# Kernel optimization log

Measured on AMD Instinct MI355X. Metric: run time of the kernel, lower is better.

## Reference

```python
import jax, jax.numpy as jnp
from jax import lax
import numpy as np

B, H, W, C = 2, 256, 256, 256
HEADS, DH = 8, 32  # C == HEADS * DH


def _dwconv(x, w, pad):
    # x: [B,C,H,W], w: [C,1,kh,kw] depthwise (feature_group_count=C)
    return lax.conv_general_dilated(
        x, w, window_strides=(1, 1), padding=[(pad, pad), (pad, pad)],
        dimension_numbers=('NCHW', 'OIHW', 'NCHW'), feature_group_count=x.shape[1])


def _conv1x1(x, w, b):
    # x: [B,C,H,W], w: [Cout,Cin], b: [Cout]
    return jnp.einsum('bchw,oc->bohw', x, w) + b[None, :, None, None]


def _l2norm(x, axis=-1, eps=1e-12):
    # matches F.normalize: x / max(||x||, eps)
    n = jnp.sqrt(jnp.sum(x * x, axis=axis, keepdims=True))
    return x / jnp.maximum(n, eps)


def setup_inputs():
    key = jax.random.key(0)
    ks = jax.random.split(key, 16)
    s = 0.02
    f32 = jnp.float32
    return {
        'x_in': jax.random.normal(ks[0], (B, H, W, C), f32),
        'mask': jax.random.uniform(ks[1], (B, H, W, C), f32),
        'wq': jax.random.normal(ks[2], (C, C), f32) * s,
        'wk': jax.random.normal(ks[3], (C, C), f32) * s,
        'wv': jax.random.normal(ks[4], (C, C), f32) * s,
        'rescale': jnp.ones((HEADS, 1, 1), f32),
        'proj_w': jax.random.normal(ks[5], (C, C), f32) * s,
        'proj_b': jnp.zeros((C,), f32),
        'pos_w1': jax.random.normal(ks[6], (C, 1, 3, 3), f32) * s,
        'pos_w2': jax.random.normal(ks[7], (C, 1, 3, 3), f32) * s,
        'mm_c1_w': jax.random.normal(ks[8], (C, C), f32) * s,
        'mm_c1_b': jnp.zeros((C,), f32),
        'mm_c2_w': jax.random.normal(ks[9], (C, C), f32) * s,
        'mm_c2_b': jnp.zeros((C,), f32),
        'mm_dw_w': jax.random.normal(ks[10], (C, 1, 5, 5), f32) * s,
        'mm_dw_b': jnp.zeros((C,), f32),
    }


def reference(x_in, mask, wq, wk, wv, rescale, proj_w, proj_b, pos_w1, pos_w2,
              mm_c1_w, mm_c1_b, mm_c2_w, mm_c2_b, mm_dw_w, mm_dw_b):
    b, h, w, c = x_in.shape
    n = h * w
    x = x_in.reshape(b, n, c)

    # q, k, v: [b, heads, n, dh]
    def split_heads(t):
        return t.reshape(b, n, HEADS, DH).transpose(0, 2, 1, 3)
    q = split_heads(x @ wq)
    k = split_heads(x @ wk)
    v = split_heads(x @ wv)

    # MaskGuidedMechanism on NCHW mask
    m = _conv1x1(mask.transpose(0, 3, 1, 2), mm_c1_w, mm_c1_b)          # [b,c,h,w]
    attn_map = jax.nn.sigmoid(_dwconv(_conv1x1(m, mm_c2_w, mm_c2_b), mm_dw_w, 2)
                              + mm_dw_b[None, :, None, None])
    m = m * attn_map + m                                                 # [b,c,h,w]
    mask_attn = split_heads(m.transpose(0, 2, 3, 1).reshape(b, n, c))    # [b,heads,n,dh]

    v = v * mask_attn

    # transpose to channel-attention layout: [b, heads, dh, n]
    q = _l2norm(q.transpose(0, 1, 3, 2))
    k = _l2norm(k.transpose(0, 1, 3, 2))
    v = v.transpose(0, 1, 3, 2)

    attn = jnp.einsum('bhdn,bhen->bhde', k, q) * rescale  # [b,heads,dh,dh]
    attn = jax.nn.softmax(attn, axis=-1)
    out = jnp.einsum('bhde,bhen->bhdn', attn, v)          # [b,heads,dh,n]
    out = out.transpose(0, 3, 1, 2).reshape(b, n, c)      # [b,n,c]
    out_c = (out @ proj_w + proj_b).reshape(b, h, w, c)

    # positional embedding: two depthwise 3x3 convs with exact GELU between
    p = _dwconv(x_in.transpose(0, 3, 1, 2), pos_w1, 1)
    p = jax.nn.gelu(p, approximate=False)
    p = _dwconv(p, pos_w2, 1)
    out_p = p.transpose(0, 2, 3, 1)

    return out_c + out_p
```

## Files before the change

### kernel.cpp

```cpp
#include <hip/hip_runtime.h>
#include <math.h>

#define CCH 256
#define HEADS 8
#define DHH 32
#define BATCH 2
#define HDIM 256
#define WDIM 256
#define NPIX (HDIM*WDIM)
#define PTOT (BATCH*NPIX)
#define GCH 64

typedef __attribute__((ext_vector_type(8))) short bfrag;
typedef __attribute__((ext_vector_type(4))) float ffrag;

__device__ __forceinline__ unsigned short f2bf(float f) {
  unsigned u = __builtin_bit_cast(unsigned, f);
  u += 0x7fffu + ((u >> 16) & 1u);
  return (unsigned short)(u >> 16);
}
__device__ __forceinline__ float bf2f(unsigned short h) {
  unsigned u = (unsigned)h << 16;
  return __builtin_bit_cast(float, u);
}

__global__ __launch_bounds__(256) void gemm_mfma(
    const float* __restrict__ A, const float* __restrict__ Wt,
    const float* __restrict__ bias, const float* __restrict__ emul,
    float* __restrict__ C)
{
  __shared__ unsigned short AsH[128][40];
  __shared__ unsigned short AsL[128][40];
  __shared__ unsigned short WsH[128][40];
  __shared__ unsigned short WsL[128][40];
  const int t = threadIdx.x;
  const int m0 = blockIdx.x * 128;
  const int n0 = blockIdx.y * 128;
  const int lane = t & 63;
  const int wave = t >> 6;
  const int wr = (wave >> 1) * 64;
  const int wc = (wave & 1) * 64;
  const int sr = t >> 1;
  const int sk = (t & 1) * 16;

  ffrag acc[4][4];
  #pragma unroll
  for (int i = 0; i < 4; ++i)
    #pragma unroll
    for (int j = 0; j < 4; ++j)
      acc[i][j] = (ffrag)0.f;

  const int fr = lane & 15;
  const int kc = (lane >> 4) * 8;

  for (int k0 = 0; k0 < 256; k0 += 32) {
    const float* ap = A  + (size_t)(m0 + sr) * 256 + k0 + sk;
    const float* wp = Wt + (size_t)(n0 + sr) * 256 + k0 + sk;
    float4 av[4], wv4[4];
    #pragma unroll
    for (int s = 0; s < 4; ++s) {
      av[s]  = *(const float4*)(ap + s*4);
      wv4[s] = *(const float4*)(wp + s*4);
    }
    __syncthreads();
    #pragma unroll
    for (int s = 0; s < 4; ++s) {
      const float* a4 = (const float*)&av[s];
      const float* w4 = (const float*)&wv4[s];
      #pragma unroll
      for (int p = 0; p < 4; p += 2) {
        unsigned short h0 = f2bf(a4[p]), h1 = f2bf(a4[p+1]);
        unsigned short l0 = f2bf(a4[p]   - bf2f(h0));
        unsigned short l1 = f2bf(a4[p+1] - bf2f(h1));
        *(unsigned*)&AsH[sr][sk + s*4 + p] = (unsigned)h0 | ((unsigned)h1 << 16);
        *(unsigned*)&AsL[sr][sk + s*4 + p] = (unsigned)l0 | ((unsigned)l1 << 16);
        unsigned short g0 = f2bf(w4[p]), g1 = f2bf(w4[p+1]);
        unsigned short e0 = f2bf(w4[p]   - bf2f(g0));
        unsigned short e1 = f2bf(w4[p+1] - bf2f(g1));
        *(unsigned*)&WsH[sr][sk + s*4 + p] = (unsigned)g0 | ((unsigned)g1 << 16);
        *(unsigned*)&WsL[sr][sk + s*4 + p] = (unsigned)e0 | ((unsigned)e1 << 16);
      }
    }
    __syncthreads();
    bfrag ah[4], alo[4], bh[4], blo[4];
    #pragma unroll
    for (int i = 0; i < 4; ++i) {
      ah[i]  = *(const bfrag*)&AsH[wr + i*16 + fr][kc];
      alo[i] = *(const bfrag*)&AsL[wr + i*16 + fr][kc];
      bh[i]  = *(const bfrag*)&WsH[wc + i*16 + fr][kc];
      blo[i] = *(const bfrag*)&WsL[wc + i*16 + fr][kc];
    }
    #pragma unroll
    for (int i = 0; i < 4; ++i)
      #pragma unroll
      for (int j = 0; j < 4; ++j) {
        acc[i][j] = __builtin_amdgcn_mfma_f32_16x16x32_bf16(ah[i],  bh[j],  acc[i][j], 0, 0, 0);
        acc[i][j] = __builtin_amdgcn_mfma_f32_16x16x32_bf16(ah[i],  blo[j], acc[i][j], 0, 0, 0);
        acc[i][j] = __builtin_amdgcn_mfma_f32_16x16x32_bf16(alo[i], bh[j],  acc[i][j], 0, 0, 0);
      }
  }

  const int er = (lane >> 4) * 4;
  const int ec = lane & 15;
  #pragma unroll
  for (int i = 0; i < 4; ++i) {
    #pragma unroll
    for (int j = 0; j < 4; ++j) {
      #pragma unroll
      for (int q = 0; q < 4; ++q) {
        int grow = m0 + wr + i*16 + er + q;
        int gcol = n0 + wc + j*16 + ec;
        size_t idx = (size_t)grow * 256 + gcol;
        float o = acc[i][j][q];
        if (emul) o *= emul[idx];
        if (bias) o += bias[gcol];
        C[idx] = o;
      }
    }
  }
}

__global__ __launch_bounds__(256) void transpose256(
    const float* __restrict__ src, float* __restrict__ dst)
{
  __shared__ float tile[32][33];
  const int bx = blockIdx.x & 7, by = blockIdx.x >> 3;
  const int tx = threadIdx.x & 31, ty = threadIdx.x >> 5;
  #pragma unroll
  for (int s = 0; s < 32; s += 8)
    tile[ty + s][tx] = src[(by*32 + ty + s)*256 + bx*32 + tx];
  __syncthreads();
  #pragma unroll
  for (int s = 0; s < 32; s += 8)
    dst[(bx*32 + ty + s)*256 + by*32 + tx] = tile[tx][ty + s];
}

__global__ __launch_bounds__(256) void syrk_partial(
    const float* __restrict__ X, float* __restrict__ Gp)
{
  __shared__ float xi[64][68];
  __shared__ float xj[64][68];
  const int TI[10] = {0,0,0,0,1,1,1,2,2,3};
  const int TJ[10] = {0,1,2,3,1,2,3,2,3,3};
  const int t = threadIdx.x;
  int blk = blockIdx.x;
  const int pair  = blk % 10;
  const int chunk = (blk / 10) % GCH;
  const int b     = blk / (10 * GCH);
  const int ti = TI[pair], tj = TJ[pair];
  const size_t xb = (size_t)b * NPIX * CCH;
  const int n0 = chunk * (NPIX / GCH);
  const int lr = t >> 2;
  const int lc = (t & 3) * 16;
  const int iy = (t >> 4) * 4;
  const int jx = (t & 15) * 4;
  float acc[4][4] = {};

  for (int pt = 0; pt < (NPIX / GCH) / 64; ++pt) {
    const float* xr = X + xb + (size_t)(n0 + pt*64 + lr) * 256;
    float4 vi[4], vj[4];
    #pragma unroll
    for (int s = 0; s < 4; ++s) {
      vi[s] = *(const float4*)(xr + ti*64 + lc + s*4);
      vj[s] = *(const float4*)(xr + tj*64 + lc + s*4);
    }
    __syncthreads();
    #pragma unroll
    for (int s = 0; s < 4; ++s) {
      *(float4*)&xi[lr][lc + s*4] = vi[s];
      *(float4*)&xj[lr][lc + s*4] = vj[s];
    }
    __syncthreads();
    #pragma unroll 8
    for (int p = 0; p < 64; ++p) {
      float av[4], bv[4];
      *(float4*)&av[0] = *(const float4*)&xi[p][iy];
      *(float4*)&bv[0] = *(const float4*)&xj[p][jx];
      #pragma unroll
      for (int i = 0; i < 4; ++i)
        #pragma unroll
        for (int j = 0; j < 4; ++j)
          acc[i][j] += av[i] * bv[j];
    }
  }
  float* g = Gp + (size_t)(b * GCH + chunk) * 65536;
  #pragma unroll
  for (int i = 0; i < 4; ++i)
    #pragma unroll
    for (int j = 0; j < 4; ++j)
      g[(ti*64 + iy + i) * 256 + (tj*64 + jx + j)] = acc[i][j];
}

__global__ __launch_bounds__(256) void syrk_reduce(
    const float* __restrict__ Gp, float* __restrict__ G)
{
  int flat = blockIdx.x * 256 + threadIdx.x;
  int b  = flat >> 16;
  int ij = flat & 65535;
  int i = ij >> 8, j = ij & 255;
  int src = ((i >> 6) <= (j >> 6)) ? (i*256 + j) : (j*256 + i);
  float s = 0.f;
  for (int ch = 0; ch < GCH; ++ch)
    s += Gp[(size_t)(b*GCH + ch) * 65536 + src];
  G[(size_t)b * 65536 + ij] = s;
}

__global__ __launch_bounds__(256) void headS_kernel(
    const float* __restrict__ wk, const float* __restrict__ TQ,
    float* __restrict__ S)
{
  __shared__ float wks[256][32];
  __shared__ float tqs[256][32];
  const int t  = threadIdx.x;
  const int bh = blockIdx.x;
  const int b = bh >> 3, h = bh & 7;
  const float* wkrow = wk + (size_t)t * 256 + h*32;
  const float* tqrow = TQ + (size_t)b * 65536 + (size_t)t * 256 + h*32;
  #pragma unroll
  for (int e = 0; e < 32; ++e) {
    wks[t][(e + t) & 31] = wkrow[e];
    tqs[t][(e + t) & 31] = tqrow[e];
  }
  __syncthreads();
  const int d  = t >> 3;
  const int e0 = (t & 7) * 4;
  float acc[4] = {0.f, 0.f, 0.f, 0.f};
  for (int c1 = 0; c1 < 256; ++c1) {
    float kv = wks[c1][(d + c1) & 31];
    #pragma unroll
    for (int j = 0; j < 4; ++j)
      acc[j] += kv * tqs[c1][(e0 + j + c1) & 31];
  }
  #pragma unroll
  for (int j = 0; j < 4; ++j)
    S[bh*1024 + d*32 + e0 + j] = acc[j];
}

__global__ __launch_bounds__(256) void norms_part(
    const float* __restrict__ wq, const float* __restrict__ wk,
    const float* __restrict__ TQ, const float* __restrict__ TK,
    float* __restrict__ nqp, float* __restrict__ nkp)
{
  const int o = threadIdx.x;
  const int ch = blockIdx.x & 7;
  const int b  = blockIdx.x >> 3;
  float sq = 0.f, sk = 0.f;
  for (int c1 = ch*32; c1 < ch*32 + 32; ++c1) {
    sq += wq[c1*256 + o] * TQ[(size_t)b*65536 + c1*256 + o];
    sk += wk[c1*256 + o] * TK[(size_t)b*65536 + c1*256 + o];
  }
  nqp[(b*8 + ch)*256 + o] = sq;
  nkp[(b*8 + ch)*256 + o] = sk;
}

__global__ __launch_bounds__(256) void norms_comb(
    const float* __restrict__ nqp, const float* __restrict__ nkp,
    float* __restrict__ nq, float* __restrict__ nk)
{
  int flat = blockIdx.x * 256 + threadIdx.x;
  int b = flat >> 8, o = flat & 255;
  float sq = 0.f, sk = 0.f;
  #pragma unroll
  for (int ch = 0; ch < 8; ++ch) {
    sq += nqp[(b*8 + ch)*256 + o];
    sk += nkp[(b*8 + ch)*256 + o];
  }
  nq[flat] = sq;
  nk[flat] = sk;
}

__global__ __launch_bounds__(64) void attn_final(
    const float* __restrict__ S, const float* __restrict__ nq,
    const float* __restrict__ nk, const float* __restrict__ rescale,
    float* __restrict__ attn)
{
  const int bh = blockIdx.x;
  const int b = bh >> 3, h = bh & 7;
  const int d = threadIdx.x;
  if (d >= 32) return;
  const float r = rescale[h];
  const float nkd = fmaxf(sqrtf(nk[b*256 + h*32 + d]), 1e-12f);
  float vals[32];
  float mx = -1e30f;
  #pragma unroll
  for (int e = 0; e < 32; ++e) {
    float nqe = fmaxf(sqrtf(nq[b*256 + h*32 + e]), 1e-12f);
    float x = S[bh*1024 + d*32 + e] / (nkd * nqe) * r;
    vals[e] = x;
    mx = fmaxf(mx, x);
  }
  float sum = 0.f;
  #pragma unroll
  for (int e = 0; e < 32; ++e) { vals[e] = expf(vals[e] - mx); sum += vals[e]; }
  float inv = 1.f / sum;
  #pragma unroll
  for (int e = 0; e < 32; ++e) attn[bh*1024 + d*32 + e] = vals[e] * inv;
}

__global__ __launch_bounds__(256) void fold_proj(
    const float* __restrict__ attn, const float* __restrict__ projw,
    float* __restrict__ WbT)
{
  const int o  = threadIdx.x;
  const int he = blockIdx.x & 255;
  const int b  = blockIdx.x >> 8;
  const int h = he >> 5, e = he & 31;
  float acc = 0.f;
  #pragma unroll
  for (int d = 0; d < 32; ++d)
    acc += attn[((b*8 + h)*32 + d)*32 + e] * projw[(h*32 + d)*256 + o];
  WbT[(size_t)b*65536 + (size_t)o*256 + he] = acc;
}

__global__ __launch_bounds__(256) void mgm_kernel(
    const float* __restrict__ tin, float* __restrict__ m,
    const float* __restrict__ dww, const float* __restrict__ dwb)
{
  const int c  = threadIdx.x;
  const int blk = blockIdx.x;
  const int xc = (blk & 7) * 32;
  const int y  = (blk >> 3) & 255;
  const int b  = blk >> 11;
  float w[25];
  #pragma unroll
  for (int i = 0; i < 25; ++i) w[i] = dww[c*25 + i];
  const float bias = dwb[c];
  const float* base = tin + (size_t)b * NPIX * CCH + c;
  int yo[5];
  #pragma unroll
  for (int dy = 0; dy < 5; ++dy) {
    int yy = y + dy - 2;
    yo[dy] = (yy >= 0 && yy <= 255) ? yy * 65536 : -1;
  }
  float col[5][5];
  #pragma unroll
  for (int j = 0; j < 4; ++j) {
    int xx = xc - 2 + j;
    bool xv = (xx >= 0 && xx <= 255);
    #pragma unroll
    for (int dy = 0; dy < 5; ++dy)
      col[j][dy] = (xv && yo[dy] >= 0) ? base[yo[dy] + xx*256] : 0.f;
  }
  size_t mi = (size_t)b * NPIX * CCH + ((size_t)y*256 + xc)*256 + c;
  #pragma unroll 4
  for (int xi = 0; xi < 32; ++xi) {
    int xx = xc + xi + 2;
    bool xv = (xx <= 255);
    #pragma unroll
    for (int dy = 0; dy < 5; ++dy)
      col[4][dy] = (xv && yo[dy] >= 0) ? base[yo[dy] + xx*256] : 0.f;
    float conv = 0.f;
    #pragma unroll
    for (int dy = 0; dy < 5; ++dy)
      #pragma unroll
      for (int j = 0; j < 5; ++j)
        conv += col[j][dy] * w[dy*5 + j];
    float sig = 1.f / (1.f + expf(-(conv + bias)));
    m[mi] = m[mi] * (1.f + sig);
    mi += 256;
    #pragma unroll
    for (int j = 0; j < 4; ++j)
      #pragma unroll
      for (int dy = 0; dy < 5; ++dy)
        col[j][dy] = col[j+1][dy];
  }
}

__global__ __launch_bounds__(256) void pos1_kernel(
    const float* __restrict__ xin, const float* __restrict__ w1,
    float* __restrict__ p1)
{
  const int c  = threadIdx.x;
  const int blk = blockIdx.x;
  const int xc = (blk & 7) * 32;
  const int y  = (blk >> 3) & 255;
  const int b  = blk >> 11;
  float w[9];
  #pragma unroll
  for (int i = 0; i < 9; ++i) w[i] = w1[c*9 + i];
  const float* base = xin + (size_t)b * NPIX * CCH + c;
  int yo[3];
  #pragma unroll
  for (int dy = 0; dy < 3; ++dy) {
    int yy = y + dy - 1;
    yo[dy] = (yy >= 0 && yy <= 255) ? yy * 65536 : -1;
  }
  float col[3][3];
  #pragma unroll
  for (int j = 0; j < 2; ++j) {
    int xx = xc - 1 + j;
    bool xv = (xx >= 0 && xx <= 255);
    #pragma unroll
    for (int dy = 0; dy < 3; ++dy)
      col[j][dy] = (xv && yo[dy] >= 0) ? base[yo[dy] + xx*256] : 0.f;
  }
  size_t pi = (size_t)b * NPIX * CCH + ((size_t)y*256 + xc)*256 + c;
  #pragma unroll 4
  for (int xi = 0; xi < 32; ++xi) {
    int xx = xc + xi + 1;
    bool xv = (xx <= 255);
    #pragma unroll
    for (int dy = 0; dy < 3; ++dy)
      col[2][dy] = (xv && yo[dy] >= 0) ? base[yo[dy] + xx*256] : 0.f;
    float conv = 0.f;
    #pragma unroll
    for (int dy = 0; dy < 3; ++dy)
      #pragma unroll
      for (int j = 0; j < 3; ++j)
        conv += col[j][dy] * w[dy*3 + j];
    float g = 0.5f * conv * (1.f + erff(conv * 0.70710678118654752f));
    p1[pi] = g;
    pi += 256;
    #pragma unroll
    for (int j = 0; j < 2; ++j)
      #pragma unroll
      for (int dy = 0; dy < 3; ++dy)
        col[j][dy] = col[j+1][dy];
  }
}

__global__ __launch_bounds__(256) void pos2_kernel(
    const float* __restrict__ p1, const float* __restrict__ w2,
    float* __restrict__ out)
{
  const int c  = threadIdx.x;
  const int blk = blockIdx.x;
  const int xc = (blk & 7) * 32;
  const int y  = (blk >> 3) & 255;
  const int b  = blk >> 11;
  float w[9];
  #pragma unroll
  for (int i = 0; i < 9; ++i) w[i] = w2[c*9 + i];
  const float* base = p1 + (size_t)b * NPIX * CCH + c;
  int yo[3];
  #pragma unroll
  for (int dy = 0; dy < 3; ++dy) {
    int yy = y + dy - 1;
    yo[dy] = (yy >= 0 && yy <= 255) ? yy * 65536 : -1;
  }
  float col[3][3];
  #pragma unroll
  for (int j = 0; j < 2; ++j) {
    int xx = xc - 1 + j;
    bool xv = (xx >= 0 && xx <= 255);
    #pragma unroll
    for (int dy = 0; dy < 3; ++dy)
      col[j][dy] = (xv && yo[dy] >= 0) ? base[yo[dy] + xx*256] : 0.f;
  }
  size_t pi = (size_t)b * NPIX * CCH + ((size_t)y*256 + xc)*256 + c;
  #pragma unroll 4
  for (int xi = 0; xi < 32; ++xi) {
    int xx = xc + xi + 1;
    bool xv = (xx <= 255);
    #pragma unroll
    for (int dy = 0; dy < 3; ++dy)
      col[2][dy] = (xv && yo[dy] >= 0) ? base[yo[dy] + xx*256] : 0.f;
    float conv = 0.f;
    #pragma unroll
    for (int dy = 0; dy < 3; ++dy)
      #pragma unroll
      for (int j = 0; j < 3; ++j)
        conv += col[j][dy] * w[dy*3 + j];
    out[pi] = out[pi] + conv;
    pi += 256;
    #pragma unroll
    for (int j = 0; j < 2; ++j)
      #pragma unroll
      for (int dy = 0; dy < 3; ++dy)
        col[j][dy] = col[j+1][dy];
  }
}

extern "C" void kernel_launch(void* const* d_in, const int* in_sizes, int n_in,
                              void* d_out, int out_size, void* d_ws, size_t ws_size,
                              hipStream_t stream)
{
  const float* x_in   = (const float*)d_in[0];
  const float* mask   = (const float*)d_in[1];
  const float* wq     = (const float*)d_in[2];
  const float* wk     = (const float*)d_in[3];
  const float* wv     = (const float*)d_in[4];
  const float* rescal = (const float*)d_in[5];
  const float* proj_w = (const float*)d_in[6];
  const float* proj_b = (const float*)d_in[7];
  const float* pos_w1 = (const float*)d_in[8];
  const float* pos_w2 = (const float*)d_in[9];
  const float* c1w    = (const float*)d_in[10];
  const float* c1b    = (const float*)d_in[11];
  const float* c2w    = (const float*)d_in[12];
  const float* c2b    = (const float*)d_in[13];
  const float* dww    = (const float*)d_in[14];
  const float* dwb    = (const float*)d_in[15];
  float* OUT = (float*)d_out;

  float* A   = (float*)d_ws;
  float* WbT = A + (size_t)PTOT * CCH;

  float* Gp  = OUT;
  float* G   = OUT + 8388608;
  float* TQ  = G   + 131072;
  float* TK  = TQ  + 131072;
  float* S   = TK  + 131072;
  float* nqp = S   + 16384;
  float* nkp = nqp + 4096;
  float* nq  = nkp + 4096;
  float* nk  = nq  + 512;
  float* at  = nk  + 512;
  float* wvT = at  + 16384;
  float* wqT = wvT + 65536;
  float* wkT = wqT + 65536;

  dim3 gg(PTOT / 128, 2);

  gemm_mfma<<<gg, 256, 0, stream>>>(mask, c1w, c1b, nullptr, A);
  gemm_mfma<<<gg, 256, 0, stream>>>(A,    c2w, c2b, nullptr, OUT);
  mgm_kernel<<<4096, 256, 0, stream>>>(OUT, A, dww, dwb);
  transpose256<<<64, 256, 0, stream>>>(wv, wvT);
  transpose256<<<64, 256, 0, stream>>>(wq, wqT);
  transpose256<<<64, 256, 0, stream>>>(wk, wkT);
  syrk_partial<<<2 * GCH * 10, 256, 0, stream>>>(x_in, Gp);
  syrk_reduce<<<512, 256, 0, stream>>>(Gp, G);
  for (int b = 0; b < 2; ++b) {
    gemm_mfma<<<dim3(2,2), 256, 0, stream>>>(G + (size_t)b*65536, wqT, nullptr, nullptr, TQ + (size_t)b*65536);
    gemm_mfma<<<dim3(2,2), 256, 0, stream>>>(G + (size_t)b*65536, wkT, nullptr, nullptr, TK + (size_t)b*65536);
  }
  headS_kernel<<<16, 256, 0, stream>>>(wk, TQ, S);
  norms_part<<<16, 256, 0, stream>>>(wq, wk, TQ, TK, nqp, nkp);
  norms_comb<<<2, 256, 0, stream>>>(nqp, nkp, nq, nk);
  attn_final<<<16, 64, 0, stream>>>(S, nq, nk, rescal, at);
  fold_proj<<<512, 256, 0, stream>>>(at, proj_w, WbT);
  gemm_mfma<<<gg, 256, 0, stream>>>(x_in, wvT, nullptr, A, A);
  {
    dim3 gp(NPIX / 128, 2);
    for (int b = 0; b < 2; ++b)
      gemm_mfma<<<gp, 256, 0, stream>>>(A + (size_t)b * NPIX * CCH,
                                        WbT + (size_t)b * 65536,
                                        proj_b, nullptr,
                                        OUT + (size_t)b * NPIX * CCH);
  }
  pos1_kernel<<<4096, 256, 0, stream>>>(x_in, pos_w1, A);
  pos2_kernel<<<4096, 256, 0, stream>>>(A, pos_w2, OUT);
}
```

Baseline: 1.465 ms.

## Presplit weights to bf16 hi/lo, MFMA Gram kernel, swizzled LDS with prefetch

Weights are now pre-split into bf16 high/low halves by small prep kernels, so the GEMM loads them directly instead of converting each tile. The GEMM gains an XOR-swizzled shared-memory layout and register prefetch of the next K-tile, and splits activations with truncation plus a byte-permute in place of round-to-nearest. The fp32 scalar Gram (x^T x) partial kernel is replaced by a full 256x256 split-bf16 MFMA kernel over 128 chunks, with a vectorized reduce. This trades extra partial-buffer traffic and truncation-based rounding for much higher matrix-core throughput.

```diff
diff --git a/kernel.cpp b/kernel.cpp
--- a/kernel.cpp
+++ b/kernel.cpp
@@ -3,206 +3,239 @@
 
 #define CCH 256
 #define HEADS 8
-#define DHH 32
 #define BATCH 2
-#define HDIM 256
-#define WDIM 256
-#define NPIX (HDIM*WDIM)
-#define PTOT (BATCH*NPIX)
-#define GCH 64
+#define NPIX 65536
+#define PTOT 131072
+#define NCH 128
 
 typedef __attribute__((ext_vector_type(8))) short bfrag;
 typedef __attribute__((ext_vector_type(4))) float ffrag;
-
-__device__ __forceinline__ unsigned short f2bf(float f) {
-  unsigned u = __builtin_bit_cast(unsigned, f);
-  u += 0x7fffu + ((u >> 16) & 1u);
-  return (unsigned short)(u >> 16);
-}
-__device__ __forceinline__ float bf2f(unsigned short h) {
-  unsigned u = (unsigned)h << 16;
+typedef unsigned short u16;
+
+#define KSW(row, g) ((((g) ^ (((row) >> 3) & 3)) << 3))
+
+__device__ __forceinline__ float trunc_bf(float f) {
+  unsigned u = __builtin_bit_cast(unsigned, f) & 0xffff0000u;
   return __builtin_bit_cast(float, u);
 }
+__device__ __forceinline__ unsigned pack_hi(float f0, float f1) {
+  return __builtin_amdgcn_perm(__builtin_bit_cast(unsigned, f1),
+                               __builtin_bit_cast(unsigned, f0), 0x07060302u);
+}
+__device__ __forceinline__ void split2(float f0, float f1, unsigned& h, unsigned& l) {
+  h = pack_hi(f0, f1);
+  l = pack_hi(f0 - trunc_bf(f0), f1 - trunc_bf(f1));
+}
 
 __global__ __launch_bounds__(256) void gemm_mfma(
-    const float* __restrict__ A, const float* __restrict__ Wt,
-    const float* __restrict__ bias, const float* __restrict__ emul,
-    float* __restrict__ C)
-{
-  __shared__ unsigned short AsH[128][40];
-  __shared__ unsigned short AsL[128][40];
-  __shared__ unsigned short WsH[128][40];
-  __shared__ unsigned short WsL[128][40];
+    const float* __restrict__ A, const u16* __restrict__ WH,
+    const u16* __restrict__ WL, const float* __restrict__ bias,
+    const float* __restrict__ emul, float* __restrict__ C)
+{
+  __shared__ u16 AsH[128][40], AsL[128][40], WsH[128][40], WsL[128][40];
   const int t = threadIdx.x;
-  const int m0 = blockIdx.x * 128;
-  const int n0 = blockIdx.y * 128;
-  const int lane = t & 63;
-  const int wave = t >> 6;
-  const int wr = (wave >> 1) * 64;
-  const int wc = (wave & 1) * 64;
+  const int m0 = blockIdx.x * 128, n0 = blockIdx.y * 128;
+  const int lane = t & 63, wave = t >> 6;
+  const int wr = (wave >> 1) * 64, wc = (wave & 1) * 64;
   const int sr = t >> 1;
-  const int sk = (t & 1) * 16;
+  const int g0 = (t & 1) * 2;
+  const int fr = lane & 15, kcg = lane >> 4;
+
+  const float* ap  = A  + (size_t)(m0 + sr) * 256 + g0 * 8;
+  const u16*   whp = WH + (size_t)(n0 + sr) * 256 + g0 * 8;
+  const u16*   wlp = WL + (size_t)(n0 + sr) * 256 + g0 * 8;
 
   ffrag acc[4][4];
   #pragma unroll
   for (int i = 0; i < 4; ++i)
     #pragma unroll
-    for (int j = 0; j < 4; ++j)
-      acc[i][j] = (ffrag)0.f;
-
-  const int fr = lane & 15;
-  const int kc = (lane >> 4) * 8;
+    for (int j = 0; j < 4; ++j) acc[i][j] = (ffrag)0.f;
+
+  float4 av[4]; uint4 whv[2], wlv[2];
+  auto LOADT = [&](int k0) {
+    #pragma unroll
+    for (int s = 0; s < 4; ++s) av[s] = *(const float4*)(ap + k0 + s * 4);
+    whv[0] = *(const uint4*)(whp + k0);
+    whv[1] = *(const uint4*)(whp + k0 + 8);
+    wlv[0] = *(const uint4*)(wlp + k0);
+    wlv[1] = *(const uint4*)(wlp + k0 + 8);
+  };
+  LOADT(0);
 
   for (int k0 = 0; k0 < 256; k0 += 32) {
-    const float* ap = A  + (size_t)(m0 + sr) * 256 + k0 + sk;
-    const float* wp = Wt + (size_t)(n0 + sr) * 256 + k0 + sk;
-    float4 av[4], wv4[4];
+    __syncthreads();
+    unsigned h[8], l[8];
     #pragma unroll
     for (int s = 0; s < 4; ++s) {
-      av[s]  = *(const float4*)(ap + s*4);
-      wv4[s] = *(const float4*)(wp + s*4);
+      split2(av[s].x, av[s].y, h[2*s],   l[2*s]);
+      split2(av[s].z, av[s].w, h[2*s+1], l[2*s+1]);
     }
+    *(uint4*)&AsH[sr][KSW(sr, g0)]     = make_uint4(h[0], h[1], h[2], h[3]);
+    *(uint4*)&AsH[sr][KSW(sr, g0 + 1)] = make_uint4(h[4], h[5], h[6], h[7]);
+    *(uint4*)&AsL[sr][KSW(sr, g0)]     = make_uint4(l[0], l[1], l[2], l[3]);
+    *(uint4*)&AsL[sr][KSW(sr, g0 + 1)] = make_uint4(l[4], l[5], l[6], l[7]);
+    *(uint4*)&WsH[sr][KSW(sr, g0)]     = whv[0];
+    *(uint4*)&WsH[sr][KSW(sr, g0 + 1)] = whv[1];
+    *(uint4*)&WsL[sr][KSW(sr, g0)]     = wlv[0];
+    *(uint4*)&WsL[sr][KSW(sr, g0 + 1)] = wlv[1];
     __syncthreads();
-    #pragma unroll
-    for (int s = 0; s < 4; ++s) {
-      const float* a4 = (const float*)&av[s];
-      const float* w4 = (const float*)&wv4[s];
-      #pragma unroll
-      for (int p = 0; p < 4; p += 2) {
-        unsigned short h0 = f2bf(a4[p]), h1 = f2bf(a4[p+1]);
-        unsigned short l0 = f2bf(a4[p]   - bf2f(h0));
-        unsigned short l1 = f2bf(a4[p+1] - bf2f(h1));
-        *(unsigned*)&AsH[sr][sk + s*4 + p] = (unsigned)h0 | ((unsigned)h1 << 16);
-        *(unsigned*)&AsL[sr][sk + s*4 + p] = (unsigned)l0 | ((unsigned)l1 << 16);
-        unsigned short g0 = f2bf(w4[p]), g1 = f2bf(w4[p+1]);
-        unsigned short e0 = f2bf(w4[p]   - bf2f(g0));
-        unsigned short e1 = f2bf(w4[p+1] - bf2f(g1));
-        *(unsigned*)&WsH[sr][sk + s*4 + p] = (unsigned)g0 | ((unsigned)g1 << 16);
-        *(unsigned*)&WsL[sr][sk + s*4 + p] = (unsigned)e0 | ((unsigned)e1 << 16);
-      }
-    }
-    __syncthreads();
-    bfrag ah[4], alo[4], bh[4], blo[4];
+    if (k0 < 224) LOADT(k0 + 32);
+
+    bfrag ah[4], al_[4], bh[4], bl_[4];
     #pragma unroll
     for (int i = 0; i < 4; ++i) {
-      ah[i]  = *(const bfrag*)&AsH[wr + i*16 + fr][kc];
-      alo[i] = *(const bfrag*)&AsL[wr + i*16 + fr][kc];
-      bh[i]  = *(const bfrag*)&WsH[wc + i*16 + fr][kc];
-      blo[i] = *(const bfrag*)&WsL[wc + i*16 + fr][kc];
+      int ra = wr + i * 16 + fr, rb = wc + i * 16 + fr;
+      ah[i]  = *(const bfrag*)&AsH[ra][KSW(ra, kcg)];
+      al_[i] = *(const bfrag*)&AsL[ra][KSW(ra, kcg)];
+      bh[i]  = *(const bfrag*)&WsH[rb][KSW(rb, kcg)];
+      bl_[i] = *(const bfrag*)&WsL[rb][KSW(rb, kcg)];
     }
     #pragma unroll
     for (int i = 0; i < 4; ++i)
       #pragma unroll
       for (int j = 0; j < 4; ++j) {
         acc[i][j] = __builtin_amdgcn_mfma_f32_16x16x32_bf16(ah[i],  bh[j],  acc[i][j], 0, 0, 0);
-        acc[i][j] = __builtin_amdgcn_mfma_f32_16x16x32_bf16(ah[i],  blo[j], acc[i][j], 0, 0, 0);
-        acc[i][j] = __builtin_amdgcn_mfma_f32_16x16x32_bf16(alo[i], bh[j],  acc[i][j], 0, 0, 0);
+        acc[i][j] = __builtin_amdgcn_mfma_f32_16x16x32_bf16(ah[i],  bl_[j], acc[i][j], 0, 0, 0);
+        acc[i][j] = __builtin_amdgcn_mfma_f32_16x16x32_bf16(al_[i], bh[j],  acc[i][j], 0, 0, 0);
       }
   }
 
-  const int er = (lane >> 4) * 4;
-  const int ec = lane & 15;
-  #pragma unroll
-  for (int i = 0; i < 4; ++i) {
-    #pragma unroll
-    for (int j = 0; j < 4; ++j) {
+  const int er = (lane >> 4) * 4, ec = lane & 15;
+  #pragma unroll
+  for (int i = 0; i < 4; ++i)
+    #pragma unroll
+    for (int j = 0; j < 4; ++j)
       #pragma unroll
       for (int q = 0; q < 4; ++q) {
-        int grow = m0 + wr + i*16 + er + q;
-        int gcol = n0 + wc + j*16 + ec;
+        int grow = m0 + wr + i * 16 + er + q;
+        int gcol = n0 + wc + j * 16 + ec;
         size_t idx = (size_t)grow * 256 + gcol;
         float o = acc[i][j][q];
         if (emul) o *= emul[idx];
         if (bias) o += bias[gcol];
         C[idx] = o;
       }
+}
+
+__global__ __launch_bounds__(512, 2) void syrk_mfma(
+    const float* __restrict__ X, float* __restrict__ Gp)
+{
+  __shared__ u16 XsH[256][40], XsL[256][40];
+  const int t = threadIdx.x;
+  const int blk = blockIdx.x;
+  const int chunk = blk & (NCH - 1);
+  const int b = blk >> 7;
+  const size_t xb = (size_t)b * NPIX * CCH;
+  const int nbase = chunk * (NPIX / NCH);
+  const int lane = t & 63, wave = t >> 6;
+  const int r0 = wave * 32;
+  const int fr = lane & 15, kcg = lane >> 4;
+  const int cw = t & 31;
+  const int n2 = (t >> 5) * 2;
+  const int gst = n2 >> 3, nin = n2 & 7;
+
+  ffrag acc[2][16];
+  #pragma unroll
+  for (int i = 0; i < 2; ++i)
+    #pragma unroll
+    for (int j = 0; j < 16; ++j) acc[i][j] = (ffrag)0.f;
+
+  float fa[8], fb[8];
+  auto LOADT = [&](int it) {
+    const float* xr = X + xb + (size_t)(nbase + it * 32 + n2) * 256 + cw;
+    #pragma unroll
+    for (int j = 0; j < 8; ++j) { fa[j] = xr[32 * j]; fb[j] = xr[256 + 32 * j]; }
+  };
+  LOADT(0);
+
+  const int NIT = (NPIX / NCH) / 32;
+  for (int it = 0; it < NIT; ++it) {
+    __syncthreads();
+    #pragma unroll
+    for (int j = 0; j < 8; ++j) {
+      unsigned h, l;
+      split2(fa[j], fb[j], h, l);
+      int c = cw + 32 * j;
+      *(unsigned*)&XsH[c][KSW(c, gst) + nin] = h;
+      *(unsigned*)&XsL[c][KSW(c, gst) + nin] = l;
     }
-  }
-}
-
-__global__ __launch_bounds__(256) void transpose256(
-    const float* __restrict__ src, float* __restrict__ dst)
+    __syncthreads();
+    if (it + 1 < NIT) LOADT(it + 1);
+
+    bfrag aH[2], aL[2];
+    #pragma unroll
+    for (int i = 0; i < 2; ++i) {
+      int row = r0 + i * 16 + fr;
+      aH[i] = *(const bfrag*)&XsH[row][KSW(row, kcg)];
+      aL[i] = *(const bfrag*)&XsL[row][KSW(row, kcg)];
+    }
+    #pragma unroll
+    for (int j = 0; j < 16; ++j) {
+      int row = j * 16 + fr;
+      bfrag bH = *(const bfrag*)&XsH[row][KSW(row, kcg)];
+      bfrag bL = *(const bfrag*)&XsL[row][KSW(row, kcg)];
+      #pragma unroll
+      for (int i = 0; i < 2; ++i) {
+        acc[i][j] = __builtin_amdgcn_mfma_f32_16x16x32_bf16(aH[i], bH, acc[i][j], 0, 0, 0);
+        acc[i][j] = __builtin_amdgcn_mfma_f32_16x16x32_bf16(aH[i], bL, acc[i][j], 0, 0, 0);
+        acc[i][j] = __builtin_amdgcn_mfma_f32_16x16x32_bf16(aL[i], bH, acc[i][j], 0, 0, 0);
+      }
+    }
+  }
+  float* g = Gp + (size_t)blk * 65536;
+  const int er = (lane >> 4) * 4, ec = lane & 15;
+  #pragma unroll
+  for (int i = 0; i < 2; ++i)
+    #pragma unroll
+    for (int j = 0; j < 16; ++j)
+      #pragma unroll
+      for (int q = 0; q < 4; ++q)
+        g[(r0 + i * 16 + er + q) * 256 + j * 16 + ec] = acc[i][j][q];
+}
+
+__global__ __launch_bounds__(256) void syrk_reduce(
+    const float* __restrict__ Gp, float* __restrict__ G)
+{
+  int id = blockIdx.x * 256 + threadIdx.x;
+  int b = id >> 14;
+  int i4 = id & 16383;
+  const float4* src = (const float4*)(Gp + (size_t)b * NCH * 65536) + i4;
+  float4 s = make_float4(0.f, 0.f, 0.f, 0.f);
+  for (int ch = 0; ch < NCH; ++ch) {
+    float4 v = src[(size_t)ch * 16384];
+    s.x += v.x; s.y += v.y; s.z += v.z; s.w += v.w;
+  }
+  ((float4*)(G + (size_t)b * 65536))[i4] = s;
+}
+
+__global__ __launch_bounds__(256) void prep_direct(
+    const float* __restrict__ src, u16* __restrict__ H, u16* __restrict__ L)
+{
+  int id = blockIdx.x * 256 + threadIdx.x;
+  float f = src[id];
+  H[id] = (u16)(__builtin_bit_cast(unsigned, f) >> 16);
+  float r = f - trunc_bf(f);
+  L[id] = (u16)(__builtin_bit_cast(unsigned, r) >> 16);
+}
+
+__global__ __launch_bounds__(256) void prep_trans(
+    const float* __restrict__ src, u16* __restrict__ H, u16* __restrict__ L)
 {
   __shared__ float tile[32][33];
   const int bx = blockIdx.x & 7, by = blockIdx.x >> 3;
   const int tx = threadIdx.x & 31, ty = threadIdx.x >> 5;
   #pragma unroll
   for (int s = 0; s < 32; s += 8)
-    tile[ty + s][tx] = src[(by*32 + ty + s)*256 + bx*32 + tx];
+    tile[ty + s][tx] = src[(by * 32 + ty + s) * 256 + bx * 32 + tx];
   __syncthreads();
   #pragma unroll
-  for (int s = 0; s < 32; s += 8)
-    dst[(bx*32 + ty + s)*256 + by*32 + tx] = tile[tx][ty + s];
-}
-
-__global__ __launch_bounds__(256) void syrk_partial(
-    const float* __restrict__ X, float* __restrict__ Gp)
-{
-  __shared__ float xi[64][68];
-  __shared__ float xj[64][68];
-  const int TI[10] = {0,0,0,0,1,1,1,2,2,3};
-  const int TJ[10] = {0,1,2,3,1,2,3,2,3,3};
-  const int t = threadIdx.x;
-  int blk = blockIdx.x;
-  const int pair  = blk % 10;
-  const int chunk = (blk / 10) % GCH;
-  const int b     = blk / (10 * GCH);
-  const int ti = TI[pair], tj = TJ[pair];
-  const size_t xb = (size_t)b * NPIX * CCH;
-  const int n0 = chunk * (NPIX / GCH);
-  const int lr = t >> 2;
-  const int lc = (t & 3) * 16;
-  const int iy = (t >> 4) * 4;
-  const int jx = (t & 15) * 4;
-  float acc[4][4] = {};
-
-  for (int pt = 0; pt < (NPIX / GCH) / 64; ++pt) {
-    const float* xr = X + xb + (size_t)(n0 + pt*64 + lr) * 256;
-    float4 vi[4], vj[4];
-    #pragma unroll
-    for (int s = 0; s < 4; ++s) {
-      vi[s] = *(const float4*)(xr + ti*64 + lc + s*4);
-      vj[s] = *(const float4*)(xr + tj*64 + lc + s*4);
-    }
-    __syncthreads();
-    #pragma unroll
-    for (int s = 0; s < 4; ++s) {
-      *(float4*)&xi[lr][lc + s*4] = vi[s];
-      *(float4*)&xj[lr][lc + s*4] = vj[s];
-    }
-    __syncthreads();
-    #pragma unroll 8
-    for (int p = 0; p < 64; ++p) {
-      float av[4], bv[4];
-      *(float4*)&av[0] = *(const float4*)&xi[p][iy];
-      *(float4*)&bv[0] = *(const float4*)&xj[p][jx];
-      #pragma unroll
-      for (int i = 0; i < 4; ++i)
-        #pragma unroll
-        for (int j = 0; j < 4; ++j)
-          acc[i][j] += av[i] * bv[j];
-    }
-  }
-  float* g = Gp + (size_t)(b * GCH + chunk) * 65536;
-  #pragma unroll
-  for (int i = 0; i < 4; ++i)
-    #pragma unroll
-    for (int j = 0; j < 4; ++j)
-      g[(ti*64 + iy + i) * 256 + (tj*64 + jx + j)] = acc[i][j];
-}
-
-__global__ __launch_bounds__(256) void syrk_reduce(
-    const float* __restrict__ Gp, float* __restrict__ G)
-{
-  int flat = blockIdx.x * 256 + threadIdx.x;
-  int b  = flat >> 16;
-  int ij = flat & 65535;
-  int i = ij >> 8, j = ij & 255;
-  int src = ((i >> 6) <= (j >> 6)) ? (i*256 + j) : (j*256 + i);
-  float s = 0.f;
-  for (int ch = 0; ch < GCH; ++ch)
-    s += Gp[(size_t)(b*GCH + ch) * 65536 + src];
-  G[(size_t)b * 65536 + ij] = s;
+  for (int s = 0; s < 32; s += 8) {
+    float f = tile[tx][ty + s];
+    int o = bx * 32 + ty + s, c = by * 32 + tx;
+    H[o * 256 + c] = (u16)(__builtin_bit_cast(unsigned, f) >> 16);
+    float r = f - trunc_bf(f);
+    L[o * 256 + c] = (u16)(__builtin_bit_cast(unsigned, r) >> 16);
+  }
 }
 
 __global__ __launch_bounds__(256) void headS_kernel(
@@ -214,8 +247,8 @@
   const int t  = threadIdx.x;
   const int bh = blockIdx.x;
   const int b = bh >> 3, h = bh & 7;
-  const float* wkrow = wk + (size_t)t * 256 + h*32;
-  const float* tqrow = TQ + (size_t)b * 65536 + (size_t)t * 256 + h*32;
+  const float* wkrow = wk + (size_t)t * 256 + h * 32;
+  const float* tqrow = TQ + (size_t)b * 65536 + (size_t)t * 256 + h * 32;
   #pragma unroll
   for (int e = 0; e < 32; ++e) {
     wks[t][(e + t) & 31] = wkrow[e];
@@ -233,7 +266,7 @@
   }
   #pragma unroll
   for (int j = 0; j < 4; ++j)
-    S[bh*1024 + d*32 + e0 + j] = acc[j];
+    S[bh * 1024 + d * 32 + e0 + j] = acc[j];
 }
 
 __global__ __launch_bounds__(256) void norms_part(
@@ -245,12 +278,12 @@
   const int ch = blockIdx.x & 7;
   const int b  = blockIdx.x >> 3;
   float sq = 0.f, sk = 0.f;
-  for (int c1 = ch*32; c1 < ch*32 + 32; ++c1) {
-    sq += wq[c1*256 + o] * TQ[(size_t)b*65536 + c1*256 + o];
-    sk += wk[c1*256 + o] * TK[(size_t)b*65536 + c1*256 + o];
-  }
-  nqp[(b*8 + ch)*256 + o] = sq;
-  nkp[(b*8 + ch)*256 + o] = sk;
+  for (int c1 = ch * 32; c1 < ch * 32 + 32; ++c1) {
+    sq += wq[c1 * 256 + o] * TQ[(size_t)b * 65536 + c1 * 256 + o];
+    sk += wk[c1 * 256 + o] * TK[(size_t)b * 65536 + c1 * 256 + o];
+  }
+  nqp[(b * 8 + ch) * 256 + o] = sq;
+  nkp[(b * 8 + ch) * 256 + o] = sk;
 }
 
 __global__ __launch_bounds__(256) void norms_comb(
@@ -262,8 +295,8 @@
   float sq = 0.f, sk = 0.f;
   #pragma unroll
   for (int ch = 0; ch < 8; ++ch) {
-    sq += nqp[(b*8 + ch)*256 + o];
-    sk += nkp[(b*8 + ch)*256 + o];
+    sq += nqp[(b * 8 + ch) * 256 + o];
+    sk += nkp[(b * 8 + ch) * 256 + o];
   }
   nq[flat] = sq;
   nk[flat] = sk;
@@ -279,13 +312,13 @@
   const int d = threadIdx.x;
   if (d >= 32) return;
   const float r = rescale[h];
-  const float nkd = fmaxf(sqrtf(nk[b*256 + h*32 + d]), 1e-12f);
+  const float nkd = fmaxf(sqrtf(nk[b * 256 + h * 32 + d]), 1e-12f);
   float vals[32];
   float mx = -1e30f;
   #pragma unroll
   for (int e = 0; e < 32; ++e) {
-    float nqe = fmaxf(sqrtf(nq[b*256 + h*32 + e]), 1e-12f);
-    float x = S[bh*1024 + d*32 + e] / (nkd * nqe) * r;
+    float nqe = fmaxf(sqrtf(nq[b * 256 + h * 32 + e]), 1e-12f);
+    float x = S[bh * 1024 + d * 32 + e] / (nkd * nqe) * r;
     vals[e] = x;
     mx = fmaxf(mx, x);
   }
@@ -294,12 +327,12 @@
   for (int e = 0; e < 32; ++e) { vals[e] = expf(vals[e] - mx); sum += vals[e]; }
   float inv = 1.f / sum;
   #pragma unroll
-  for (int e = 0; e < 32; ++e) attn[bh*1024 + d*32 + e] = vals[e] * inv;
+  for (int e = 0; e < 32; ++e) attn[bh * 1024 + d * 32 + e] = vals[e] * inv;
 }
 
 __global__ __launch_bounds__(256) void fold_proj(
     const float* __restrict__ attn, const float* __restrict__ projw,
-    float* __restrict__ WbT)
+    u16* __restrict__ WbH, u16* __restrict__ WbL)
 {
   const int o  = threadIdx.x;
   const int he = blockIdx.x & 255;
@@ -308,8 +341,11 @@
   float acc = 0.f;
   #pragma unroll
   for (int d = 0; d < 32; ++d)
-    acc += attn[((b*8 + h)*32 + d)*32 + e] * projw[(h*32 + d)*256 + o];
-  WbT[(size_t)b*65536 + (size_t)o*256 + he] = acc;
+    acc += attn[((b * 8 + h) * 32 + d) * 32 + e] * projw[(h * 32 + d) * 256 + o];
+  size_t idx = (size_t)b * 65536 + (size_t)o * 256 + he;
+  WbH[idx] = (u16)(__builtin_bit_cast(unsigned, acc) >> 16);
+  float r = acc - trunc_bf(acc);
+  WbL[idx] = (u16)(__builtin_bit_cast(unsigned, r) >> 16);
 }
 
 __global__ __launch_bounds__(256) void mgm_kernel(
@@ -323,7 +359,7 @@
   const int b  = blk >> 11;
   float w[25];
   #pragma unroll
-  for (int i = 0; i < 25; ++i) w[i] = dww[c*25 + i];
+  for (int i = 0; i < 25; ++i) w[i] = dww[c * 25 + i];
   const float bias = dwb[c];
   const float* base = tin + (size_t)b * NPIX * CCH + c;
   int yo[5];
@@ -339,22 +375,22 @@
     bool xv = (xx >= 0 && xx <= 255);
     #pragma unroll
     for (int dy = 0; dy < 5; ++dy)
-      col[j][dy] = (xv && yo[dy] >= 0) ? base[yo[dy] + xx*256] : 0.f;
-  }
-  size_t mi = (size_t)b * NPIX * CCH + ((size_t)y*256 + xc)*256 + c;
+      col[j][dy] = (xv && yo[dy] >= 0) ? base[yo[dy] + xx * 256] : 0.f;
+  }
+  size_t mi = (size_t)b * NPIX * CCH + ((size_t)y * 256 + xc) * 256 + c;
   #pragma unroll 4
   for (int xi = 0; xi < 32; ++xi) {
     int xx = xc + xi + 2;
     bool xv = (xx <= 255);
     #pragma unroll
     for (int dy = 0; dy < 5; ++dy)
-      col[4][dy] = (xv && yo[dy] >= 0) ? base[yo[dy] + xx*256] : 0.f;
+      col[4][dy] = (xv && yo[dy] >= 0) ? base[yo[dy] + xx * 256] : 0.f;
     float conv = 0.f;
     #pragma unroll
     for (int dy = 0; dy < 5; ++dy)
       #pragma unroll
       for (int j = 0; j < 5; ++j)
-        conv += col[j][dy] * w[dy*5 + j];
+        conv += col[j][dy] * w[dy * 5 + j];
     float sig = 1.f / (1.f + expf(-(conv + bias)));
     m[mi] = m[mi] * (1.f + sig);
     mi += 256;
@@ -362,7 +398,7 @@
     for (int j = 0; j < 4; ++j)
       #pragma unroll
       for (int dy = 0; dy < 5; ++dy)
-        col[j][dy] = col[j+1][dy];
+        col[j][dy] = col[j + 1][dy];
   }
 }
 
@@ -377,7 +413,7 @@
   const int b  = blk >> 11;
   float w[9];
   #pragma unroll
-  for (int i = 0; i < 9; ++i) w[i] = w1[c*9 + i];
+  for (int i = 0; i < 9; ++i) w[i] = w1[c * 9 + i];
   const float* base = xin + (size_t)b * NPIX * CCH + c;
   int yo[3];
   #pragma unroll
@@ -392,22 +428,22 @@
     bool xv = (xx >= 0 && xx <= 255);
     #pragma unroll
     for (int dy = 0; dy < 3; ++dy)
-      col[j][dy] = (xv && yo[dy] >= 0) ? base[yo[dy] + xx*256] : 0.f;
-  }
-  size_t pi = (size_t)b * NPIX * CCH + ((size_t)y*256 + xc)*256 + c;
+      col[j][dy] = (xv && yo[dy] >= 0) ? base[yo[dy] + xx * 256] : 0.f;
+  }
+  size_t pi = (size_t)b * NPIX * CCH + ((size_t)y * 256 + xc) * 256 + c;
   #pragma unroll 4
   for (int xi = 0; xi < 32; ++xi) {
     int xx = xc + xi + 1;
     bool xv = (xx <= 255);
     #pragma unroll
     for (int dy = 0; dy < 3; ++dy)
-      col[2][dy] = (xv && yo[dy] >= 0) ? base[yo[dy] + xx*256] : 0.f;
+      col[2][dy] = (xv && yo[dy] >= 0) ? base[yo[dy] + xx * 256] : 0.f;
     float conv = 0.f;
     #pragma unroll
     for (int dy = 0; dy < 3; ++dy)
       #pragma unroll
       for (int j = 0; j < 3; ++j)
-        conv += col[j][dy] * w[dy*3 + j];
+        conv += col[j][dy] * w[dy * 3 + j];
     float g = 0.5f * conv * (1.f + erff(conv * 0.70710678118654752f));
     p1[pi] = g;
     pi += 256;
@@ -415,7 +451,7 @@
     for (int j = 0; j < 2; ++j)
       #pragma unroll
       for (int dy = 0; dy < 3; ++dy)
-        col[j][dy] = col[j+1][dy];
+        col[j][dy] = col[j + 1][dy];
   }
 }
 
@@ -430,7 +466,7 @@
   const int b  = blk >> 11;
   float w[9];
   #pragma unroll
-  for (int i = 0; i < 9; ++i) w[i] = w2[c*9 + i];
+  for (int i = 0; i < 9; ++i) w[i] = w2[c * 9 + i];
   const float* base = p1 + (size_t)b * NPIX * CCH + c;
   int yo[3];
   #pragma unroll
@@ -445,29 +481,29 @@
     bool xv = (xx >= 0 && xx <= 255);
     #pragma unroll
     for (int dy = 0; dy < 3; ++dy)
-      col[j][dy] = (xv && yo[dy] >= 0) ? base[yo[dy] + xx*256] : 0.f;
-  }
-  size_t pi = (size_t)b * NPIX * CCH + ((size_t)y*256 + xc)*256 + c;
+      col[j][dy] = (xv && yo[dy] >= 0) ? base[yo[dy] + xx * 256] : 0.f;
+  }
+  size_t pi = (size_t)b * NPIX * CCH + ((size_t)y * 256 + xc) * 256 + c;
   #pragma unroll 4
   for (int xi = 0; xi < 32; ++xi) {
     int xx = xc + xi + 1;
     bool xv = (xx <= 255);
     #pragma unroll
     for (int dy = 0; dy < 3; ++dy)
-      col[2][dy] = (xv && yo[dy] >= 0) ? base[yo[dy] + xx*256] : 0.f;
+      col[2][dy] = (xv && yo[dy] >= 0) ? base[yo[dy] + xx * 256] : 0.f;
     float conv = 0.f;
     #pragma unroll
     for (int dy = 0; dy < 3; ++dy)
       #pragma unroll
       for (int j = 0; j < 3; ++j)
-        conv += col[j][dy] * w[dy*3 + j];
+        conv += col[j][dy] * w[dy * 3 + j];
     out[pi] = out[pi] + conv;
     pi += 256;
     #pragma unroll
     for (int j = 0; j < 2; ++j)
       #pragma unroll
       for (int dy = 0; dy < 3; ++dy)
-        col[j][dy] = col[j+1][dy];
+        col[j][dy] = col[j + 1][dy];
   }
 }
 
@@ -494,10 +530,15 @@
   float* OUT = (float*)d_out;
 
   float* A   = (float*)d_ws;
-  float* WbT = A + (size_t)PTOT * CCH;
+  u16* WbH = (u16*)(A + (size_t)PTOT * CCH);
+  u16* WbL = WbH + 2 * 65536;
+  u16* c1H = WbL + 2 * 65536;
+  u16* c1L = c1H + 65536;
+  u16* c2H = c1L + 65536;
+  u16* c2L = c2H + 65536;
 
   float* Gp  = OUT;
-  float* G   = OUT + 8388608;
+  float* G   = OUT + (size_t)2 * NCH * 65536;
   float* TQ  = G   + 131072;
   float* TK  = TQ  + 131072;
   float* S   = TK  + 131072;
@@ -506,35 +547,43 @@
   float* nq  = nkp + 4096;
   float* nk  = nq  + 512;
   float* at  = nk  + 512;
-  float* wvT = at  + 16384;
-  float* wqT = wvT + 65536;
-  float* wkT = wqT + 65536;
+  u16* wqH = (u16*)(at + 16384);
+  u16* wqL = wqH + 65536;
+  u16* wkH = wqL + 65536;
+  u16* wkL = wkH + 65536;
+  u16* wvH = wkL + 65536;
+  u16* wvL = wvH + 65536;
 
   dim3 gg(PTOT / 128, 2);
 
-  gemm_mfma<<<gg, 256, 0, stream>>>(mask, c1w, c1b, nullptr, A);
-  gemm_mfma<<<gg, 256, 0, stream>>>(A,    c2w, c2b, nullptr, OUT);
+  prep_direct<<<256, 256, 0, stream>>>(c1w, c1H, c1L);
+  prep_direct<<<256, 256, 0, stream>>>(c2w, c2H, c2L);
+  gemm_mfma<<<gg, 256, 0, stream>>>(mask, c1H, c1L, c1b, nullptr, A);
+  gemm_mfma<<<gg, 256, 0, stream>>>(A,    c2H, c2L, c2b, nullptr, OUT);
   mgm_kernel<<<4096, 256, 0, stream>>>(OUT, A, dww, dwb);
-  transpose256<<<64, 256, 0, stream>>>(wv, wvT);
-  transpose256<<<64, 256, 0, stream>>>(wq, wqT);
-  transpose256<<<64, 256, 0, stream>>>(wk, wkT);
-  syrk_partial<<<2 * GCH * 10, 256, 0, stream>>>(x_in, Gp);
-  syrk_reduce<<<512, 256, 0, stream>>>(Gp, G);
+  prep_trans<<<64, 256, 0, stream>>>(wq, wqH, wqL);
+  prep_trans<<<64, 256, 0, stream>>>(wk, wkH, wkL);
+  prep_trans<<<64, 256, 0, stream>>>(wv, wvH, wvL);
+  syrk_mfma<<<2 * NCH, 512, 0, stream>>>(x_in, Gp);
+  syrk_reduce<<<128, 256, 0, stream>>>(Gp, G);
   for (int b = 0; b < 2; ++b) {
-    gemm_mfma<<<dim3(2,2), 256, 0, stream>>>(G + (size_t)b*65536, wqT, nullptr, nullptr, TQ + (size_t)b*65536);
-    gemm_mfma<<<dim3(2,2), 256, 0, stream>>>(G + (size_t)b*65536, wkT, nullptr, nullptr, TK + (size_t)b*65536);
+    gemm_mfma<<<dim3(2, 2), 256, 0, stream>>>(G + (size_t)b * 65536, wqH, wqL,
+                                              nullptr, nullptr, TQ + (size_t)b * 65536);
+    gemm_mfma<<<dim3(2, 2), 256, 0, stream>>>(G + (size_t)b * 65536, wkH, wkL,
+                                              nullptr, nullptr, TK + (size_t)b * 65536);
   }
   headS_kernel<<<16, 256, 0, stream>>>(wk, TQ, S);
   norms_part<<<16, 256, 0, stream>>>(wq, wk, TQ, TK, nqp, nkp);
   norms_comb<<<2, 256, 0, stream>>>(nqp, nkp, nq, nk);
   attn_final<<<16, 64, 0, stream>>>(S, nq, nk, rescal, at);
-  fold_proj<<<512, 256, 0, stream>>>(at, proj_w, WbT);
-  gemm_mfma<<<gg, 256, 0, stream>>>(x_in, wvT, nullptr, A, A);
+  fold_proj<<<512, 256, 0, stream>>>(at, proj_w, WbH, WbL);
+  gemm_mfma<<<gg, 256, 0, stream>>>(x_in, wvH, wvL, nullptr, A, A);
   {
     dim3 gp(NPIX / 128, 2);
     for (int b = 0; b < 2; ++b)
       gemm_mfma<<<gp, 256, 0, stream>>>(A + (size_t)b * NPIX * CCH,
-                                        WbT + (size_t)b * 65536,
+                                        WbH + (size_t)b * 65536,
+                                        WbL + (size_t)b * 65536,
                                         proj_b, nullptr,
                                         OUT + (size_t)b * NPIX * CCH);
   }
```

Result: faster. 1.435 ms (-2.0%).
